# Kernel tuning notes

Hardware: AMD Instinct MI355X
Metric: run time of the kernel (lower is better)

Reference implementation:

```python
import jax, jax.numpy as jnp
import numpy as np


def setup_inputs() -> dict:
    key = jax.random.key(0)
    k1, k2 = jax.random.split(key)
    B, C, H, W = 64, 2048, 16, 16
    P = 200
    x = jax.random.normal(k1, (B, C, H, W), dtype=jnp.float32)
    prototype_vectors = jax.random.normal(k2, (P, C), dtype=jnp.float32)
    return {"x": x, "prototype_vectors": prototype_vectors}


def reference(x, prototype_vectors):
    # x: (B, C, H, W); prototypes: (P, C)
    B, C, H, W = x.shape
    P = prototype_vectors.shape[0]
    x_flat = x.reshape(B, C, H * W)                      # (B, C, S)
    # broadcasted (B,P,C,S) subtraction; same math, GEMM for cross term)
    x_sq = jnp.sum(x_flat * x_flat, axis=1)              # (B, S)
    p_sq = jnp.sum(prototype_vectors * prototype_vectors, axis=1)  # (P,)
    cross = jnp.einsum('pc,bcs->bps', prototype_vectors, x_flat)   # (B, P, S)
    distances = x_sq[:, None, :] + p_sq[None, :, None] - 2.0 * cross  # (B, P, S)
    similarities = -distances
    max_similarities = jnp.max(similarities, axis=2)     # (B, P)
    activation_maps = similarities.reshape(B, P, H, W)   # (B, P, H, W)
    return max_similarities, distances, activation_maps
```

## Files before the change

### kernel.cpp

```cpp
#include <hip/hip_runtime.h>

typedef float floatx4 __attribute__((ext_vector_type(4)));
typedef unsigned int uintx4 __attribute__((ext_vector_type(4)));
typedef unsigned short ushortx4 __attribute__((ext_vector_type(4)));
typedef __bf16 bf16x8 __attribute__((ext_vector_type(8)));

#define B_ 64
#define C_ 2048
#define S_ 256
#define P_ 200
#define PM_ 256
#define ST_ 64
#define BK_ 64
#define NKT_ 32

__device__ __forceinline__ unsigned short f2bf(float f) {
  unsigned int u = __float_as_uint(f);
  u += 0x7FFFu + ((u >> 16) & 1u);
  return (unsigned short)(u >> 16);
}

__global__ void __launch_bounds__(256) prep_kernel(const float* __restrict__ proto,
                                                   unsigned short* __restrict__ wsp,
                                                   float* __restrict__ wpsq) {
  const int r = blockIdx.x;
  const int t = threadIdx.x;
  float s = 0.f;
#pragma unroll
  for (int rep = 0; rep < 2; ++rep) {
    const int c = rep * 1024 + t * 4;
    floatx4 v = {0.f, 0.f, 0.f, 0.f};
    if (r < P_) v = *reinterpret_cast<const floatx4*>(&proto[r * C_ + c]);
    ushortx4 h;
#pragma unroll
    for (int i = 0; i < 4; ++i) { s += v[i] * v[i]; h[i] = f2bf(v[i]); }
    *reinterpret_cast<ushortx4*>(&wsp[r * C_ + c]) = h;
  }
#pragma unroll
  for (int o = 32; o > 0; o >>= 1) s += __shfl_down(s, o);
  __shared__ float red[4];
  if ((t & 63) == 0) red[t >> 6] = s;
  __syncthreads();
  if (t == 0) wpsq[r] = red[0] + red[1] + red[2] + red[3];
}

__global__ void __launch_bounds__(512, 2) main_kernel(const float* __restrict__ x,
    const unsigned short* __restrict__ wsp, const float* __restrict__ wpsq,
    float* __restrict__ out_dist, float* __restrict__ out_act,
    float* __restrict__ wpmax) {
  __shared__ unsigned short As[2][16384];
  __shared__ unsigned short Bs[2][4096];
  __shared__ float xsq_lds[512];
  __shared__ float xsqf[64];
  __shared__ float psq_lds[256];
  __shared__ float pmax_lds[512];

  const int t = threadIdx.x;
  const int lane = t & 63;
  const int w = t >> 6;
  const int wm = w >> 1, wn = w & 1;
  const int lg = lane >> 4, l15 = lane & 15;
  const int b = blockIdx.x >> 2, st = blockIdx.x & 3;
  const int s0 = st << 6;

  if (t < 256) psq_lds[t] = wpsq[t];

  const int sg = t & 15;
  const int kc0 = t >> 4;

  const float* xb = x + (size_t)b * C_ * S_ + s0 + 4 * sg;

  floatx4 acc[4][2] = {};
  float xsq4[4] = {0.f, 0.f, 0.f, 0.f};

#pragma unroll
  for (int q = 0; q < 4; ++q) {
    const int g2 = q * 512 + t;
    const int m = g2 >> 3, kb = g2 & 7;
    uintx4 av = *reinterpret_cast<const uintx4*>(&wsp[m * C_ + kb * 8]);
    const int dst = ((m >> 4) << 10) + (kb << 7) + ((m & 15) << 3);
    *reinterpret_cast<uintx4*>(&As[0][dst]) = av;
  }
#pragma unroll
  for (int rep = 0; rep < 2; ++rep) {
    const int kc = rep * 32 + kc0;
    floatx4 xv = *reinterpret_cast<const floatx4*>(&xb[(size_t)kc * S_]);
#pragma unroll
    for (int i = 0; i < 4; ++i) {
      xsq4[i] += xv[i] * xv[i];
      const int n = 4 * sg + i;
      Bs[0][((n >> 4) << 10) + ((kc >> 3) << 7) + ((n & 15) << 3) + (kc & 7)] = f2bf(xv[i]);
    }
  }
  __syncthreads();

  int cur = 0;
  for (int kt = 0; kt < NKT_; ++kt) {
    uintx4 av[4];
    floatx4 xv[2];
    const bool has = (kt + 1 < NKT_);
    if (has) {
      const int ktile = (kt + 1) << 6;
#pragma unroll
      for (int q = 0; q < 4; ++q) {
        const int g2 = q * 512 + t;
        const int m = g2 >> 3, kb = g2 & 7;
        av[q] = *reinterpret_cast<const uintx4*>(&wsp[m * C_ + ktile + kb * 8]);
      }
#pragma unroll
      for (int rep = 0; rep < 2; ++rep) {
        const int kc = rep * 32 + kc0;
        xv[rep] = *reinterpret_cast<const floatx4*>(&xb[(size_t)(ktile + kc) * S_]);
      }
    }
#pragma unroll
    for (int ks = 0; ks < 2; ++ks) {
      bf16x8 afr[4], bfr[2];
#pragma unroll
      for (int mi = 0; mi < 4; ++mi) {
        const int idx = ((wm * 4 + mi) << 10) + ((ks * 4 + lg) << 7) + (l15 << 3);
        afr[mi] = *reinterpret_cast<const bf16x8*>(&As[cur][idx]);
      }
#pragma unroll
      for (int ni = 0; ni < 2; ++ni) {
        const int idx = ((wn * 2 + ni) << 10) + ((ks * 4 + lg) << 7) + (l15 << 3);
        bfr[ni] = *reinterpret_cast<const bf16x8*>(&Bs[cur][idx]);
      }
#pragma unroll
      for (int mi = 0; mi < 4; ++mi)
#pragma unroll
        for (int ni = 0; ni < 2; ++ni)
          acc[mi][ni] = __builtin_amdgcn_mfma_f32_16x16x32_bf16(afr[mi], bfr[ni], acc[mi][ni], 0, 0, 0);
    }
    if (has) {
      const int nb = cur ^ 1;
#pragma unroll
      for (int q = 0; q < 4; ++q) {
        const int g2 = q * 512 + t;
        const int m = g2 >> 3, kb = g2 & 7;
        const int dst = ((m >> 4) << 10) + (kb << 7) + ((m & 15) << 3);
        *reinterpret_cast<uintx4*>(&As[nb][dst]) = av[q];
      }
#pragma unroll
      for (int rep = 0; rep < 2; ++rep) {
        const int kc = rep * 32 + kc0;
#pragma unroll
        for (int i = 0; i < 4; ++i) {
          const float f = xv[rep][i];
          xsq4[i] += f * f;
          const int n = 4 * sg + i;
          Bs[nb][((n >> 4) << 10) + ((kc >> 3) << 7) + ((n & 15) << 3) + (kc & 7)] = f2bf(f);
        }
      }
    }
    __syncthreads();
    cur ^= 1;
  }

#pragma unroll
  for (int i = 0; i < 4; ++i) {
    float v = xsq4[i];
    v += __shfl_xor(v, 16);
    v += __shfl_xor(v, 32);
    xsq4[i] = v;
  }
  if (lane < 16) {
#pragma unroll
    for (int i = 0; i < 4; ++i) xsq_lds[w * 64 + lane * 4 + i] = xsq4[i];
  }
  __syncthreads();
  if (t < 64) {
    float s = 0.f;
#pragma unroll
    for (int w2 = 0; w2 < 8; ++w2) s += xsq_lds[w2 * 64 + t];
    xsqf[t] = s;
  }
  __syncthreads();

#pragma unroll
  for (int mi = 0; mi < 4; ++mi) {
#pragma unroll
    for (int r = 0; r < 4; ++r) {
      const int m = wm * 64 + mi * 16 + lg * 4 + r;
      const float ps = psq_lds[m];
      float rowmax = -3.0e38f;
#pragma unroll
      for (int ni = 0; ni < 2; ++ni) {
        const int n = wn * 32 + ni * 16 + l15;
        const float d = xsqf[n] + ps - 2.0f * acc[mi][ni][r];
        if (m < P_) {
          const int gi = ((b * P_ + m) << 8) + s0 + n;
          out_dist[gi] = d;
          out_act[gi] = -d;
        }
        rowmax = fmaxf(rowmax, -d);
      }
#pragma unroll
      for (int off = 1; off < 16; off <<= 1)
        rowmax = fmaxf(rowmax, __shfl_xor(rowmax, off));
      if (l15 == 0) pmax_lds[wn * 256 + m] = rowmax;
    }
  }
  __syncthreads();
  if (t < 256) {
    const float v = fmaxf(pmax_lds[t], pmax_lds[256 + t]);
    wpmax[(((b << 8) + t) << 2) + st] = v;
  }
}

__global__ void __launch_bounds__(256) fin_kernel(const float* __restrict__ wpmax,
                                                  float* __restrict__ out_max) {
  const int i = blockIdx.x * 256 + threadIdx.x;
  if (i >= B_ * P_) return;
  const int b = i / P_;
  const int p = i - b * P_;
  floatx4 v = *reinterpret_cast<const floatx4*>(&wpmax[((b << 8) + p) << 2]);
  out_max[i] = fmaxf(fmaxf(v[0], v[1]), fmaxf(v[2], v[3]));
}

extern "C" void kernel_launch(void* const* d_in, const int* in_sizes, int n_in,
                              void* d_out, int out_size, void* d_ws, size_t ws_size,
                              hipStream_t stream) {
  (void)in_sizes; (void)n_in; (void)out_size; (void)ws_size;
  const float* x = (const float*)d_in[0];
  const float* proto = (const float*)d_in[1];
  float* out = (float*)d_out;

  unsigned short* wsp = (unsigned short*)d_ws;
  float* wpsq  = (float*)((char*)d_ws + (size_t)PM_ * C_ * 2);
  float* wpmax = (float*)((char*)d_ws + (size_t)PM_ * C_ * 2 + 1024);

  float* out_max  = out;
  float* out_dist = out + B_ * P_;
  float* out_act  = out + B_ * P_ + B_ * P_ * S_;

  prep_kernel<<<PM_, 256, 0, stream>>>(proto, wsp, wpsq);
  main_kernel<<<B_ * (S_ / ST_), 512, 0, stream>>>(x, wsp, wpsq, out_dist, out_act, wpmax);
  fin_kernel<<<(B_ * P_ + 255) / 256, 256, 0, stream>>>(wpmax, out_max);
}
```

Before: 242.8 us.

## Pre-tile prototypes in LDS order and stream them with direct global-to-LDS loads

The prep kernel now writes the bf16 prototype matrix already in the per-k-tile LDS fragment layout. This lets the main kernel copy it with global_load_lds instead of staging it through registers. The spatial tile shrinks from 64 to 32 columns, giving 512 blocks, and launch bounds rise to 4 blocks per CU to improve occupancy. The x tile uses an XOR-swizzled LDS layout, and the epilogue writes per-block row maxima directly without an LDS reduction. The tradeoff is that prototype tiles are re-read by twice as many blocks, and the 72KB of LDS per block may prevent reaching the intended occupancy.

```diff
diff --git a/kernel.cpp b/kernel.cpp
--- a/kernel.cpp
+++ b/kernel.cpp
@@ -1,7 +1,6 @@
 #include <hip/hip_runtime.h>
 
 typedef float floatx4 __attribute__((ext_vector_type(4)));
-typedef unsigned int uintx4 __attribute__((ext_vector_type(4)));
 typedef unsigned short ushortx4 __attribute__((ext_vector_type(4)));
 typedef __bf16 bf16x8 __attribute__((ext_vector_type(8)));
 
@@ -10,8 +9,8 @@
 #define S_ 256
 #define P_ 200
 #define PM_ 256
-#define ST_ 64
-#define BK_ 64
+#define ST_ 32
+#define NST_ 8
 #define NKT_ 32
 
 __device__ __forceinline__ unsigned short f2bf(float f) {
@@ -25,17 +24,22 @@
                                                    float* __restrict__ wpsq) {
   const int r = blockIdx.x;
   const int t = threadIdx.x;
+  floatx4 v0 = {0.f,0.f,0.f,0.f}, v1 = {0.f,0.f,0.f,0.f};
+  if (r < P_) {
+    v0 = *reinterpret_cast<const floatx4*>(proto + (size_t)r * C_ + t * 8);
+    v1 = *reinterpret_cast<const floatx4*>(proto + (size_t)r * C_ + t * 8 + 4);
+  }
   float s = 0.f;
-#pragma unroll
-  for (int rep = 0; rep < 2; ++rep) {
-    const int c = rep * 1024 + t * 4;
-    floatx4 v = {0.f, 0.f, 0.f, 0.f};
-    if (r < P_) v = *reinterpret_cast<const floatx4*>(&proto[r * C_ + c]);
-    ushortx4 h;
-#pragma unroll
-    for (int i = 0; i < 4; ++i) { s += v[i] * v[i]; h[i] = f2bf(v[i]); }
-    *reinterpret_cast<ushortx4*>(&wsp[r * C_ + c]) = h;
-  }
+  ushortx4 h0, h1;
+#pragma unroll
+  for (int i = 0; i < 4; ++i) {
+    s += v0[i]*v0[i] + v1[i]*v1[i];
+    h0[i] = f2bf(v0[i]); h1[i] = f2bf(v1[i]);
+  }
+  const int u = (t >> 3) * 16384 + (r >> 4) * 1024 + (t & 7) * 128 + (r & 15) * 8;
+  *reinterpret_cast<ushortx4*>(wsp + u) = h0;
+  *reinterpret_cast<ushortx4*>(wsp + u + 4) = h1;
+
 #pragma unroll
   for (int o = 32; o > 0; o >>= 1) s += __shfl_down(s, o);
   __shared__ float red[4];
@@ -44,168 +48,123 @@
   if (t == 0) wpsq[r] = red[0] + red[1] + red[2] + red[3];
 }
 
-__global__ void __launch_bounds__(512, 2) main_kernel(const float* __restrict__ x,
+__global__ void __launch_bounds__(512, 4) main_kernel(const float* __restrict__ x,
     const unsigned short* __restrict__ wsp, const float* __restrict__ wpsq,
     float* __restrict__ out_dist, float* __restrict__ out_act,
     float* __restrict__ wpmax) {
-  __shared__ unsigned short As[2][16384];
-  __shared__ unsigned short Bs[2][4096];
-  __shared__ float xsq_lds[512];
-  __shared__ float xsqf[64];
-  __shared__ float psq_lds[256];
-  __shared__ float pmax_lds[512];
+  __shared__ unsigned short lds[36864];
 
   const int t = threadIdx.x;
   const int lane = t & 63;
   const int w = t >> 6;
-  const int wm = w >> 1, wn = w & 1;
   const int lg = lane >> 4, l15 = lane & 15;
-  const int b = blockIdx.x >> 2, st = blockIdx.x & 3;
-  const int s0 = st << 6;
-
-  if (t < 256) psq_lds[t] = wpsq[t];
-
-  const int sg = t & 15;
-  const int kc0 = t >> 4;
-
-  const float* xb = x + (size_t)b * C_ * S_ + s0 + 4 * sg;
-
-  floatx4 acc[4][2] = {};
-  float xsq4[4] = {0.f, 0.f, 0.f, 0.f};
+  const int b = blockIdx.x >> 3, st = blockIdx.x & 7;
+
+  const int s_ = lane & 31;
+  const int h_ = lane >> 5;
+  const float* xb = x + (size_t)b * (C_ * S_) + (size_t)(w * 8 + h_ * 4) * S_ + st * ST_ + s_;
+
+  const int slot_w = (s_ & 15) ^ ((s_ & 8) >> 1) ^ ((s_ >> 4) << 1);
+  const int wr_base = 32768 + (s_ >> 4) * 1024 + w * 128 + slot_w * 8 + h_ * 4;
+  const int slot_r0 = l15 ^ ((l15 & 8) >> 1);
+
+  floatx4 acc[2][2] = {};
+  float xsq_s = 0.f;
 
 #pragma unroll
   for (int q = 0; q < 4; ++q) {
-    const int g2 = q * 512 + t;
-    const int m = g2 >> 3, kb = g2 & 7;
-    uintx4 av = *reinterpret_cast<const uintx4*>(&wsp[m * C_ + kb * 8]);
-    const int dst = ((m >> 4) << 10) + (kb << 7) + ((m & 15) << 3);
-    *reinterpret_cast<uintx4*>(&As[0][dst]) = av;
-  }
-#pragma unroll
-  for (int rep = 0; rep < 2; ++rep) {
-    const int kc = rep * 32 + kc0;
-    floatx4 xv = *reinterpret_cast<const floatx4*>(&xb[(size_t)kc * S_]);
-#pragma unroll
-    for (int i = 0; i < 4; ++i) {
-      xsq4[i] += xv[i] * xv[i];
-      const int n = 4 * sg + i;
-      Bs[0][((n >> 4) << 10) + ((kc >> 3) << 7) + ((n & 15) << 3) + (kc & 7)] = f2bf(xv[i]);
-    }
-  }
-  __syncthreads();
-
-  int cur = 0;
+    __builtin_amdgcn_global_load_lds(
+      (const __attribute__((address_space(1))) unsigned int*)(wsp + (q * 512 + t) * 8),
+      (__attribute__((address_space(3))) unsigned int*)
+        ((__attribute__((address_space(3))) unsigned short*)lds + (q * 512 + t) * 8),
+      16, 0, 0);
+  }
+  {
+    float xj[4]; ushortx4 hv;
+#pragma unroll
+    for (int j = 0; j < 4; ++j) xj[j] = xb[j * S_];
+#pragma unroll
+    for (int j = 0; j < 4; ++j) { xsq_s += xj[j] * xj[j]; hv[j] = f2bf(xj[j]); }
+    *reinterpret_cast<ushortx4*>(&lds[wr_base]) = hv;
+  }
+  __syncthreads();
+
   for (int kt = 0; kt < NKT_; ++kt) {
-    uintx4 av[4];
-    floatx4 xv[2];
-    const bool has = (kt + 1 < NKT_);
-    if (has) {
-      const int ktile = (kt + 1) << 6;
+    const int cur = kt & 1, nb = cur ^ 1;
+    float xj[4];
+    if (kt < NKT_ - 1) {
+      const unsigned short* gsrc = wsp + (size_t)(kt + 1) * 16384;
 #pragma unroll
       for (int q = 0; q < 4; ++q) {
-        const int g2 = q * 512 + t;
-        const int m = g2 >> 3, kb = g2 & 7;
-        av[q] = *reinterpret_cast<const uintx4*>(&wsp[m * C_ + ktile + kb * 8]);
+        __builtin_amdgcn_global_load_lds(
+          (const __attribute__((address_space(1))) unsigned int*)(gsrc + (q * 512 + t) * 8),
+          (__attribute__((address_space(3))) unsigned int*)
+            ((__attribute__((address_space(3))) unsigned short*)lds + nb * 16384 + (q * 512 + t) * 8),
+          16, 0, 0);
       }
-#pragma unroll
-      for (int rep = 0; rep < 2; ++rep) {
-        const int kc = rep * 32 + kc0;
-        xv[rep] = *reinterpret_cast<const floatx4*>(&xb[(size_t)(ktile + kc) * S_]);
+      const float* xsrc = xb + (size_t)(kt + 1) * 64 * S_;
+#pragma unroll
+      for (int j = 0; j < 4; ++j) xj[j] = xsrc[j * S_];
+    }
+    {
+      const unsigned short* As_c = lds + cur * 16384;
+      const unsigned short* Bs_c = lds + 32768 + cur * 2048;
+#pragma unroll
+      for (int ks = 0; ks < 2; ++ks) {
+        const int ko = (ks * 4 + lg) * 128;
+        const bf16x8 a0 = *reinterpret_cast<const bf16x8*>(As_c + (w * 2 + 0) * 1024 + ko + l15 * 8);
+        const bf16x8 a1 = *reinterpret_cast<const bf16x8*>(As_c + (w * 2 + 1) * 1024 + ko + l15 * 8);
+        const bf16x8 b0 = *reinterpret_cast<const bf16x8*>(Bs_c + ko + slot_r0 * 8);
+        const bf16x8 b1 = *reinterpret_cast<const bf16x8*>(Bs_c + 1024 + ko + (slot_r0 ^ 2) * 8);
+        acc[0][0] = __builtin_amdgcn_mfma_f32_16x16x32_bf16(a0, b0, acc[0][0], 0, 0, 0);
+        acc[0][1] = __builtin_amdgcn_mfma_f32_16x16x32_bf16(a0, b1, acc[0][1], 0, 0, 0);
+        acc[1][0] = __builtin_amdgcn_mfma_f32_16x16x32_bf16(a1, b0, acc[1][0], 0, 0, 0);
+        acc[1][1] = __builtin_amdgcn_mfma_f32_16x16x32_bf16(a1, b1, acc[1][1], 0, 0, 0);
       }
     }
-#pragma unroll
-    for (int ks = 0; ks < 2; ++ks) {
-      bf16x8 afr[4], bfr[2];
-#pragma unroll
-      for (int mi = 0; mi < 4; ++mi) {
-        const int idx = ((wm * 4 + mi) << 10) + ((ks * 4 + lg) << 7) + (l15 << 3);
-        afr[mi] = *reinterpret_cast<const bf16x8*>(&As[cur][idx]);
+    if (kt < NKT_ - 1) {
+      ushortx4 hv;
+#pragma unroll
+      for (int j = 0; j < 4; ++j) { xsq_s += xj[j] * xj[j]; hv[j] = f2bf(xj[j]); }
+      *reinterpret_cast<ushortx4*>(&lds[wr_base + nb * 2048]) = hv;
+    }
+    __syncthreads();
+  }
+
+  float* xpart = reinterpret_cast<float*>(&lds[32768]);
+  float* xsqf  = xpart + 256;
+  {
+    const float v = xsq_s + __shfl_xor(xsq_s, 32);
+    if (lane < 32) xpart[w * 32 + lane] = v;
+  }
+  __syncthreads();
+  if (t < 32) {
+    float s2 = 0.f;
+#pragma unroll
+    for (int w2 = 0; w2 < 8; ++w2) s2 += xpart[w2 * 32 + t];
+    xsqf[t] = s2;
+  }
+  __syncthreads();
+
+  const float xn0 = xsqf[l15], xn1 = xsqf[16 + l15];
+#pragma unroll
+  for (int mi = 0; mi < 2; ++mi)
+#pragma unroll
+    for (int r = 0; r < 4; ++r) {
+      const int m = w * 32 + mi * 16 + lg * 4 + r;
+      const float ps = (m < P_) ? wpsq[m] : 0.f;
+      const float d0 = xn0 + ps - 2.0f * acc[mi][0][r];
+      const float d1 = xn1 + ps - 2.0f * acc[mi][1][r];
+      if (m < P_) {
+        const size_t gi = (size_t)(b * P_ + m) * S_ + st * ST_ + l15;
+        out_dist[gi] = d0;       out_dist[gi + 16] = d1;
+        out_act[gi]  = -d0;      out_act[gi + 16]  = -d1;
       }
-#pragma unroll
-      for (int ni = 0; ni < 2; ++ni) {
-        const int idx = ((wn * 2 + ni) << 10) + ((ks * 4 + lg) << 7) + (l15 << 3);
-        bfr[ni] = *reinterpret_cast<const bf16x8*>(&Bs[cur][idx]);
-      }
-#pragma unroll
-      for (int mi = 0; mi < 4; ++mi)
-#pragma unroll
-        for (int ni = 0; ni < 2; ++ni)
-          acc[mi][ni] = __builtin_amdgcn_mfma_f32_16x16x32_bf16(afr[mi], bfr[ni], acc[mi][ni], 0, 0, 0);
-    }
-    if (has) {
-      const int nb = cur ^ 1;
-#pragma unroll
-      for (int q = 0; q < 4; ++q) {
-        const int g2 = q * 512 + t;
-        const int m = g2 >> 3, kb = g2 & 7;
-        const int dst = ((m >> 4) << 10) + (kb << 7) + ((m & 15) << 3);
-        *reinterpret_cast<uintx4*>(&As[nb][dst]) = av[q];
-      }
-#pragma unroll
-      for (int rep = 0; rep < 2; ++rep) {
-        const int kc = rep * 32 + kc0;
-#pragma unroll
-        for (int i = 0; i < 4; ++i) {
-          const float f = xv[rep][i];
-          xsq4[i] += f * f;
-          const int n = 4 * sg + i;
-          Bs[nb][((n >> 4) << 10) + ((kc >> 3) << 7) + ((n & 15) << 3) + (kc & 7)] = f2bf(f);
-        }
-      }
-    }
-    __syncthreads();
-    cur ^= 1;
-  }
-
-#pragma unroll
-  for (int i = 0; i < 4; ++i) {
-    float v = xsq4[i];
-    v += __shfl_xor(v, 16);
-    v += __shfl_xor(v, 32);
-    xsq4[i] = v;
-  }
-  if (lane < 16) {
-#pragma unroll
-    for (int i = 0; i < 4; ++i) xsq_lds[w * 64 + lane * 4 + i] = xsq4[i];
-  }
-  __syncthreads();
-  if (t < 64) {
-    float s = 0.f;
-#pragma unroll
-    for (int w2 = 0; w2 < 8; ++w2) s += xsq_lds[w2 * 64 + t];
-    xsqf[t] = s;
-  }
-  __syncthreads();
-
-#pragma unroll
-  for (int mi = 0; mi < 4; ++mi) {
-#pragma unroll
-    for (int r = 0; r < 4; ++r) {
-      const int m = wm * 64 + mi * 16 + lg * 4 + r;
-      const float ps = psq_lds[m];
-      float rowmax = -3.0e38f;
-#pragma unroll
-      for (int ni = 0; ni < 2; ++ni) {
-        const int n = wn * 32 + ni * 16 + l15;
-        const float d = xsqf[n] + ps - 2.0f * acc[mi][ni][r];
-        if (m < P_) {
-          const int gi = ((b * P_ + m) << 8) + s0 + n;
-          out_dist[gi] = d;
-          out_act[gi] = -d;
-        }
-        rowmax = fmaxf(rowmax, -d);
-      }
-#pragma unroll
-      for (int off = 1; off < 16; off <<= 1)
-        rowmax = fmaxf(rowmax, __shfl_xor(rowmax, off));
-      if (l15 == 0) pmax_lds[wn * 256 + m] = rowmax;
-    }
-  }
-  __syncthreads();
-  if (t < 256) {
-    const float v = fmaxf(pmax_lds[t], pmax_lds[256 + t]);
-    wpmax[(((b << 8) + t) << 2) + st] = v;
-  }
+      float rm = fmaxf(-d0, -d1);
+#pragma unroll
+      for (int off = 1; off < 16; off <<= 1) rm = fmaxf(rm, __shfl_xor(rm, off));
+      if (l15 == 0 && m < P_) wpmax[(size_t)((b << 8) + m) * 8 + st] = rm;
+    }
 }
 
 __global__ void __launch_bounds__(256) fin_kernel(const float* __restrict__ wpmax,
@@ -214,8 +173,11 @@
   if (i >= B_ * P_) return;
   const int b = i / P_;
   const int p = i - b * P_;
-  floatx4 v = *reinterpret_cast<const floatx4*>(&wpmax[((b << 8) + p) << 2]);
-  out_max[i] = fmaxf(fmaxf(v[0], v[1]), fmaxf(v[2], v[3]));
+  const float* q = wpmax + (size_t)((b << 8) + p) * 8;
+  const floatx4 v0 = *reinterpret_cast<const floatx4*>(q);
+  const floatx4 v1 = *reinterpret_cast<const floatx4*>(q + 4);
+  out_max[i] = fmaxf(fmaxf(fmaxf(v0[0], v0[1]), fmaxf(v0[2], v0[3])),
+                     fmaxf(fmaxf(v1[0], v1[1]), fmaxf(v1[2], v1[3])));
 }
 
 extern "C" void kernel_launch(void* const* d_in, const int* in_sizes, int n_in,
@@ -227,14 +189,14 @@
   float* out = (float*)d_out;
 
   unsigned short* wsp = (unsigned short*)d_ws;
-  float* wpsq  = (float*)((char*)d_ws + (size_t)PM_ * C_ * 2);
-  float* wpmax = (float*)((char*)d_ws + (size_t)PM_ * C_ * 2 + 1024);
+  float* wpsq  = (float*)((char*)d_ws + (size_t)NKT_ * 16384 * 2);
+  float* wpmax = (float*)((char*)d_ws + (size_t)NKT_ * 16384 * 2 + 1024);
 
   float* out_max  = out;
   float* out_dist = out + B_ * P_;
   float* out_act  = out + B_ * P_ + B_ * P_ * S_;
 
   prep_kernel<<<PM_, 256, 0, stream>>>(proto, wsp, wpsq);
-  main_kernel<<<B_ * (S_ / ST_), 512, 0, stream>>>(x, wsp, wpsq, out_dist, out_act, wpmax);
+  main_kernel<<<B_ * NST_, 512, 0, stream>>>(x, wsp, wpsq, out_dist, out_act, wpmax);
   fin_kernel<<<(B_ * P_ + 255) / 256, 256, 0, stream>>>(wpmax, out_max);
 }
```

New measurement: 223.1 us. -8.1%, faster.
